# Kernel optimization log

Measured on AMD Instinct MI355X. Metric: run time of the kernel, lower is better.

Reference implementation:

```python
import jax, jax.numpy as jnp
import numpy as np

B, L = 16, 8192
D, NB, N, NC = 128, 6, 32, 16   # d_model, n_blocks, complex state modes (d_state//2), num_classes
E = 2 * D                       # FF expansion (expand=2)


def setup_inputs() -> dict:
    key = jax.random.key(0)
    ks = jax.random.split(key, 16)
    rn = lambda k, s, sc=0.02: jax.random.normal(k, s, jnp.float32) * sc
    return {
        "x": jax.random.normal(ks[0], (B, L, 1), jnp.float32),
        "conv_w": rn(ks[1], (D, 1, 5), 0.3),
        "conv_b": jnp.zeros((D,), jnp.float32),
        "s4_ln_w": jnp.ones((NB, D), jnp.float32),
        "s4_ln_b": jnp.zeros((NB, D), jnp.float32),
        "s4_log_dt": jax.random.uniform(ks[2], (NB, D), jnp.float32, np.log(1e-3), np.log(1e-1)),
        "s4_log_A_real": jnp.full((NB, D, N), np.log(0.5), jnp.float32),
        "s4_A_imag": jnp.ones((NB, D, 1), jnp.float32) * (np.pi * jnp.arange(N, dtype=jnp.float32)),
        "s4_C_re": rn(ks[3], (NB, D, N), 1.0),
        "s4_C_im": rn(ks[4], (NB, D, N), 1.0),
        "s4_D": rn(ks[5], (NB, D), 1.0),
        "s4_out_w": rn(ks[6], (NB, 2 * D, D)),
        "s4_out_b": jnp.zeros((NB, 2 * D), jnp.float32),
        "ff_ln_w": jnp.ones((NB, D), jnp.float32),
        "ff_ln_b": jnp.zeros((NB, D), jnp.float32),
        "ff_w1": rn(ks[7], (NB, E, D)),
        "ff_b1": jnp.zeros((NB, E), jnp.float32),
        "ff_w2": rn(ks[8], (NB, D, E)),
        "ff_b2": jnp.zeros((NB, D), jnp.float32),
        "head_w": rn(ks[9], (NC, D)),
        "head_b": jnp.zeros((NC,), jnp.float32),
    }


def _ln_c(h, w, b):
    # LayerNorm over channel dim of [B, D, L] (prenorm of ResidualBlock, transposed layout)
    mu = h.mean(1, keepdims=True)
    var = ((h - mu) ** 2).mean(1, keepdims=True)
    return (h - mu) * jax.lax.rsqrt(var + 1e-5) * w[None, :, None] + b[None, :, None]


def _s4(z, log_dt, log_A_real, A_imag, C_re, C_im, Dskip, out_w, out_b):
    # S4D diagonal SSM: ZOH-discretized kernel, FFT causal conv, GELU, GLU output projection
    Lq = z.shape[-1]
    dt = jnp.exp(log_dt)                                 # [D]
    A = -jnp.exp(log_A_real) + 1j * A_imag               # [D,N] stable diagonal
    dtA = dt[:, None] * A                                # [D,N]
    C = (C_re + 1j * C_im) * (jnp.exp(dtA) - 1.0) / A    # ZOH input discretization folded into C
    vand = jnp.exp(dtA[:, :, None] * jnp.arange(Lq))     # [D,N,L] Vandermonde of exp(dtA)
    K = 2.0 * jnp.einsum('dn,dnl->dl', C, vand).real     # [D,L] SSM convolution kernel
    nf = 2 * Lq
    y = jnp.fft.irfft(jnp.fft.rfft(z, n=nf) * jnp.fft.rfft(K, n=nf)[None], n=nf)[..., :Lq]
    y = jax.nn.gelu(y + Dskip[None, :, None] * z)        # skip term D*u then activation
    y = jnp.einsum('ed,bdl->bel', out_w, y) + out_b[None, :, None]  # position-wise d->2d
    a, g = jnp.split(y, 2, axis=1)
    return a * jax.nn.sigmoid(g)                          # GLU


def _logits(x, conv_w, conv_b, s4_ln_w, s4_ln_b, s4_log_dt, s4_log_A_real, s4_A_imag, s4_C_re, s4_C_im, s4_D, s4_out_w, s4_out_b, ff_ln_w, ff_ln_b, ff_w1, ff_b1, ff_w2, ff_b2, head_w, head_b):
    u = x.transpose(0, 2, 1)                             # [B,1,L]
    h = jax.lax.conv_general_dilated(u, conv_w, (1,), [(2, 2)], dimension_numbers=('NCH', 'OIH', 'NCH'))
    h = h + conv_b[None, :, None]                        # [B,D,L]
    nb = s4_log_dt.shape[0]
    for i in range(nb):
        z = _ln_c(h, s4_ln_w[i], s4_ln_b[i])
        h = h + _s4(z, s4_log_dt[i], s4_log_A_real[i], s4_A_imag[i], s4_C_re[i], s4_C_im[i], s4_D[i], s4_out_w[i], s4_out_b[i])
        z = _ln_c(h, ff_ln_w[i], ff_ln_b[i])
        z = jax.nn.gelu(jnp.einsum('ed,bdl->bel', ff_w1[i], z) + ff_b1[i][None, :, None])
        h = h + jnp.einsum('de,bel->bdl', ff_w2[i], z) + ff_b2[i][None, :, None]
    last = h[:, :, -1]                                   # take final timestep
    return last @ head_w.T + head_b                      # [B,NC]


def reference(x, conv_w, conv_b, s4_ln_w, s4_ln_b, s4_log_dt, s4_log_A_real, s4_A_imag, s4_C_re, s4_C_im, s4_D, s4_out_w, s4_out_b, ff_ln_w, ff_ln_b, ff_w1, ff_b1, ff_w2, ff_b2, head_w, head_b):
    logits = _logits(x, conv_w, conv_b, s4_ln_w, s4_ln_b, s4_log_dt, s4_log_A_real, s4_A_imag, s4_C_re, s4_C_im, s4_D, s4_out_w, s4_out_b, ff_ln_w, ff_ln_b, ff_w1, ff_b1, ff_w2, ff_b2, head_w, head_b)
    return jnp.argmax(logits, axis=-1)[:, None].astype(jnp.int32)
```

## Files before the change

kernel.cpp:

```cpp
#include <hip/hip_runtime.h>
#include <math.h>

#define Bb 16
#define Ls 8192
#define Dm 128
#define NBK 6
#define Nst 32
#define NCl 16
#define Em 256
#define LC 128
#define NCH 64
#define BL (Bb*Ls)

typedef __attribute__((ext_vector_type(8))) short bfrag;
typedef __attribute__((ext_vector_type(4))) float f32x4;

__device__ __forceinline__ float geluf(float x) {
    float x3 = x * x * x;
    float t = tanhf(fmaf(0.0356774081f, x3, 0.7978845608f * x));
    return 0.5f * x * (1.f + t);
}
__device__ __forceinline__ float sigmf(float x) { return 1.f / (1.f + expf(-x)); }

__device__ __forceinline__ unsigned short bf16r(float x) {
    unsigned u = __float_as_uint(x);
    return (unsigned short)((u + 0x7FFFu + ((u >> 16) & 1u)) >> 16);
}
__device__ __forceinline__ void split2(float x, unsigned short& h, unsigned short& l) {
    h = bf16r(x);
    float hf = __uint_as_float(((unsigned)h) << 16);
    l = bf16r(x - hf);
}

__global__ void s4e_conv(const float* __restrict__ x, const float* __restrict__ cw,
                         const float* __restrict__ cb, float* __restrict__ h) {
    int tid = blockIdx.x * 256 + threadIdx.x;
    int d4 = tid & 31;
    int t = tid >> 5;
    int l = t & (Ls - 1);
    int b = t >> 13;
    const float* xb = x + (size_t)b * Ls;
    float xs[5];
#pragma unroll
    for (int k = 0; k < 5; ++k) {
        int p = l + k - 2;
        xs[k] = (p >= 0 && p < Ls) ? xb[p] : 0.f;
    }
    float4 acc;
    float* ap = &acc.x;
#pragma unroll
    for (int j = 0; j < 4; ++j) {
        int d = d4 * 4 + j;
        float a = cb[d];
#pragma unroll
        for (int k = 0; k < 5; ++k) a = fmaf(cw[d * 5 + k], xs[k], a);
        ap[j] = a;
    }
    *(float4*)&h[(size_t)t * Dm + d4 * 4] = acc;
}

__global__ void s4e_lnstat(const float* __restrict__ h, float2* __restrict__ stats) {
    int tid = threadIdx.x;
    int t = blockIdx.x * 64 + (tid >> 2);
    int sub = tid & 3;
    const float* hp = h + (size_t)t * Dm + sub * 32;
    float s = 0.f, q = 0.f;
#pragma unroll
    for (int i = 0; i < 8; ++i) {
        float4 v = *(const float4*)(hp + i * 4);
        s += v.x + v.y + v.z + v.w;
        q += v.x * v.x + v.y * v.y + v.z * v.z + v.w * v.w;
    }
    s += __shfl_xor(s, 1); s += __shfl_xor(s, 2);
    q += __shfl_xor(q, 1); q += __shfl_xor(q, 2);
    float mu = s * (1.f / Dm);
    float rs = rsqrtf(q * (1.f / Dm) - mu * mu + 1e-5f);
    if (sub == 0) stats[t] = make_float2(mu, rs);
}

__global__ void s4e_setup(const float* __restrict__ log_dt, const float* __restrict__ lAr,
                          const float* __restrict__ Aim, const float* __restrict__ Cre,
                          const float* __restrict__ Cim, float2* __restrict__ wv,
                          float2* __restrict__ wp, float2* __restrict__ Cc) {
    int d = threadIdx.x;
    float dt = expf(log_dt[d]);
    for (int n = 0; n < Nst; ++n) {
        int id = d * Nst + n;
        float Ar = -expf(lAr[id]);
        float Ai = Aim[id];
        float xr = dt * Ar, xi = dt * Ai;
        float er = expf(xr);
        float wr = er * cosf(xi), wi = er * sinf(xi);
        wv[n * Dm + d] = make_float2(wr, wi);
        float den = Ar * Ar + Ai * Ai;
        float inv = 1.f / den;
        float fr = ((wr - 1.f) * Ar + wi * Ai) * inv;
        float fi = (wi * Ar - (wr - 1.f) * Ai) * inv;
        Cc[n * Dm + d] = make_float2(Cre[id] * fr - Cim[id] * fi, Cre[id] * fi + Cim[id] * fr);
        float pr = wr, pi = wi;
#pragma unroll
        for (int sq = 0; sq < 7; ++sq) {
            float nr = pr * pr - pi * pi;
            float ni = 2.f * pr * pi;
            pr = nr; pi = ni;
        }
        wp[n * Dm + d] = make_float2(pr, pi);
    }
}

__global__ void s4e_wsplit(const float* __restrict__ ow, const float* __restrict__ w1,
                           const float* __restrict__ w2, unsigned short* __restrict__ base) {
    int idx = blockIdx.x * 256 + threadIdx.x;
    int mat = idx >> 12;
    int g = idx & 4095;
    int lane = g & 63;
    int fid = g >> 6;
    int col = lane & 15, q = lane >> 4;
    const float* src;
    unsigned short *dh, *dl_;
    int rt, kt, K;
    if (mat == 0)      { src = ow; K = 128; dh = base;          dl_ = base + 32768;  rt = fid >> 2; kt = fid & 3; }
    else if (mat == 1) { src = w1; K = 128; dh = base + 65536;  dl_ = base + 98304;  rt = fid >> 2; kt = fid & 3; }
    else               { src = w2; K = 256; dh = base + 131072; dl_ = base + 163840; rt = fid >> 3; kt = fid & 7; }
    int row = rt * 16 + col;
    int k0 = kt * 32 + q * 8;
    const float* sp = src + row * K + k0;
    bfrag vh, vl;
#pragma unroll
    for (int j = 0; j < 8; ++j) {
        unsigned short hh, ll;
        split2(sp[j], hh, ll);
        vh[j] = (short)hh; vl[j] = (short)ll;
    }
    *(bfrag*)&dh[g * 8] = vh;
    *(bfrag*)&dl_[g * 8] = vl;
}

__global__ __launch_bounds__(256) void s4e_s1(const float* __restrict__ h,
        const float2* __restrict__ stats, const float* __restrict__ lnw,
        const float* __restrict__ lnb, const float2* __restrict__ wv,
        float2* __restrict__ send) {
    int tid = blockIdx.x * 256 + threadIdx.x;
    int dl = tid & 31;
    int m  = (tid >> 5) & 1;
    int dh = (tid >> 6) & 3;
    int c  = (tid >> 8) & (NCH - 1);
    int b  = tid >> 14;
    int d  = dh * 32 + dl;
    int n0 = m * 16;
    float wr[16], wi[16], sr[16], si[16];
#pragma unroll
    for (int k = 0; k < 16; ++k) {
        float2 t = wv[(n0 + k) * Dm + d];
        wr[k] = t.x; wi[k] = t.y; sr[k] = 0.f; si[k] = 0.f;
    }
    float wd = lnw[d], bd = lnb[d];
    const float* hp = h + ((size_t)b * Ls + c * LC) * Dm + d;
    const float2* st = stats + (size_t)b * Ls + c * LC;
#pragma unroll 4
    for (int j = 0; j < LC; ++j) {
        float2 sj = st[j];
        float zv = (hp[(size_t)j * Dm] - sj.x) * sj.y * wd + bd;
#pragma unroll
        for (int k = 0; k < 16; ++k) {
            float t = fmaf(-wi[k], si[k], zv);
            float nr = fmaf(wr[k], sr[k], t);
            float ni = fmaf(wi[k], sr[k], wr[k] * si[k]);
            sr[k] = nr; si[k] = ni;
        }
    }
    float2* o = send + ((size_t)(b * NCH + c) * Nst + n0) * Dm + d;
#pragma unroll
    for (int k = 0; k < 16; ++k) o[k * Dm] = make_float2(sr[k], si[k]);
}

__global__ void s4e_s2(const float2* __restrict__ wp, float2* __restrict__ s) {
    int tid = blockIdx.x * 256 + threadIdx.x;
    int d = tid & 127;
    int n = (tid >> 7) & 31;
    int b = tid >> 12;
    float2 W = wp[n * Dm + d];
    float Sr = 0.f, Si = 0.f;
    size_t base = ((size_t)(b * NCH) * Nst + n) * Dm + d;
    size_t cs = (size_t)Nst * Dm;
    for (int c0 = 0; c0 < NCH; c0 += 8) {
        float2 E[8];
#pragma unroll
        for (int k = 0; k < 8; ++k) E[k] = s[base + (size_t)(c0 + k) * cs];
#pragma unroll
        for (int k = 0; k < 8; ++k) {
            float2 o = make_float2(Sr, Si);
            float nr = fmaf(W.x, Sr, fmaf(-W.y, Si, E[k].x));
            float ni = fmaf(W.x, Si, fmaf(W.y, Sr, E[k].y));
            Sr = nr; Si = ni;
            s[base + (size_t)(c0 + k) * cs] = o;
        }
    }
}

__global__ __launch_bounds__(256) void s4e_s3(const float* __restrict__ h,
        const float2* __restrict__ stats, const float* __restrict__ lnw,
        const float* __restrict__ lnb, const float2* __restrict__ wv,
        const float2* __restrict__ Cc, const float2* __restrict__ sinit,
        const float* __restrict__ Dsk,
        unsigned short* __restrict__ acth, unsigned short* __restrict__ actl) {
    int tid = blockIdx.x * 256 + threadIdx.x;
    int dl = tid & 31;
    int m  = (tid >> 5) & 1;
    int dh = (tid >> 6) & 3;
    int c  = (tid >> 8) & (NCH - 1);
    int b  = tid >> 14;
    int d  = dh * 32 + dl;
    int n0 = m * 16;
    float wr[16], wi[16], cr[16], ci[16], sr[16], si[16];
    const float2* s0 = sinit + ((size_t)(b * NCH + c) * Nst + n0) * Dm + d;
#pragma unroll
    for (int k = 0; k < 16; ++k) {
        float2 t = wv[(n0 + k) * Dm + d];  wr[k] = t.x; wi[k] = t.y;
        float2 cc = Cc[(n0 + k) * Dm + d]; cr[k] = cc.x; ci[k] = cc.y;
        float2 ss = s0[k * Dm];            sr[k] = ss.x; si[k] = ss.y;
    }
    float wd = lnw[d], bd = lnb[d];
    float Dv = Dsk[d];
    size_t ib = ((size_t)b * Ls + c * LC) * Dm + d;
    const float2* st = stats + (size_t)b * Ls + c * LC;
#pragma unroll 2
    for (int j = 0; j < LC; ++j) {
        float2 sj = st[j];
        float zv = (h[ib + (size_t)j * Dm] - sj.x) * sj.y * wd + bd;
        float acc = 0.f;
#pragma unroll
        for (int k = 0; k < 16; ++k) {
            float t = fmaf(-wi[k], si[k], zv);
            float nr = fmaf(wr[k], sr[k], t);
            float ni = fmaf(wi[k], sr[k], wr[k] * si[k]);
            sr[k] = nr; si[k] = ni;
            acc = fmaf(cr[k], nr, acc);
            acc = fmaf(-ci[k], ni, acc);
        }
        acc += __shfl_xor(acc, 32);
        float av = geluf(fmaf(Dv, zv, 2.f * acc));
        unsigned short hh, ll;
        split2(av, hh, ll);
        if (m == 0) {
            acth[ib + (size_t)j * Dm] = hh;
            actl[ib + (size_t)j * Dm] = ll;
        }
    }
}

__global__ __launch_bounds__(256) void s4e_outproj(const unsigned short* __restrict__ acth,
        const unsigned short* __restrict__ actl, const unsigned short* __restrict__ wsp,
        const float* __restrict__ bias, float* __restrict__ h) {
    __shared__ __align__(16) unsigned short smem[8192];
    unsigned short* Ah = smem;
    unsigned short* Al = smem + 4096;
    float* Rf = (float*)smem;
    const unsigned short* Whi = wsp;
    const unsigned short* Wlo = wsp + 32768;
    size_t l0 = (size_t)blockIdx.x * 32;
    int tid = threadIdx.x;
    {
        const unsigned short* gh = acth + l0 * Dm;
        const unsigned short* gl = actl + l0 * Dm;
        for (int i = tid * 8; i < 32 * 128; i += 2048) {
            int r = i >> 7;
            int di = i ^ ((r & 7) << 3);
            *(bfrag*)&Ah[di] = *(const bfrag*)&gh[i];
            *(bfrag*)&Al[di] = *(const bfrag*)&gl[i];
        }
    }
    __syncthreads();
    int w = tid >> 6, lane = tid & 63;
    int col = lane & 15, q = lane >> 4;
    f32x4 acc[2][4];
#pragma unroll
    for (int m = 0; m < 2; ++m)
#pragma unroll
        for (int nt = 0; nt < 4; ++nt) acc[m][nt] = (f32x4){0.f, 0.f, 0.f, 0.f};
#pragma unroll
    for (int ks = 0; ks < 4; ++ks) {
        int kb = ks * 32 + q * 8;
        int i0 = (col * 128 + kb) ^ ((col & 7) << 3);
        int i1 = ((16 + col) * 128 + kb) ^ ((col & 7) << 3);
        bfrag a0h = *(bfrag*)&Ah[i0], a0l = *(bfrag*)&Al[i0];
        bfrag a1h = *(bfrag*)&Ah[i1], a1l = *(bfrag*)&Al[i1];
#pragma unroll
        for (int nt = 0; nt < 4; ++nt) {
            int rt = (nt < 2) ? (w * 2 + nt) : (8 + w * 2 + (nt - 2));
            int off = ((rt * 4 + ks) * 64 + lane) * 8;
            bfrag bh = *(const bfrag*)&Whi[off];
            bfrag bl = *(const bfrag*)&Wlo[off];
            acc[0][nt] = __builtin_amdgcn_mfma_f32_16x16x32_bf16(a0h, bh, acc[0][nt], 0, 0, 0);
            acc[0][nt] = __builtin_amdgcn_mfma_f32_16x16x32_bf16(a0h, bl, acc[0][nt], 0, 0, 0);
            acc[0][nt] = __builtin_amdgcn_mfma_f32_16x16x32_bf16(a0l, bh, acc[0][nt], 0, 0, 0);
            acc[1][nt] = __builtin_amdgcn_mfma_f32_16x16x32_bf16(a1h, bh, acc[1][nt], 0, 0, 0);
            acc[1][nt] = __builtin_amdgcn_mfma_f32_16x16x32_bf16(a1h, bl, acc[1][nt], 0, 0, 0);
            acc[1][nt] = __builtin_amdgcn_mfma_f32_16x16x32_bf16(a1l, bh, acc[1][nt], 0, 0, 0);
        }
    }
    __syncthreads();
#pragma unroll
    for (int m = 0; m < 2; ++m)
#pragma unroll
        for (int nt = 0; nt < 2; ++nt) {
            int dout = w * 32 + nt * 16 + col;
            float ba = bias[dout], bg = bias[dout + 128];
#pragma unroll
            for (int r = 0; r < 4; ++r) {
                int l = m * 16 + q * 4 + r;
                float a = acc[m][nt][r] + ba;
                float g = acc[m][nt + 2][r] + bg;
                Rf[l * 128 + dout] = a * sigmf(g);
            }
        }
    __syncthreads();
    size_t gb = l0 * Dm + (size_t)tid * 16;
#pragma unroll
    for (int i = 0; i < 4; ++i) {
        float4 r = *(float4*)&Rf[tid * 16 + i * 4];
        float4 hv = *(float4*)&h[gb + i * 4];
        hv.x += r.x; hv.y += r.y; hv.z += r.z; hv.w += r.w;
        *(float4*)&h[gb + i * 4] = hv;
    }
}

__global__ __launch_bounds__(256) void s4e_ffk(const float* __restrict__ lnw,
        const float* __restrict__ lnb, const unsigned short* __restrict__ wsp,
        const float* __restrict__ b1, const float* __restrict__ b2, float* __restrict__ h) {
    __shared__ __align__(16) unsigned short smem[24576];
    unsigned short* Zh = smem;
    unsigned short* Zl = smem + 4096;
    unsigned short* Eh = smem + 8192;
    unsigned short* El = smem + 16384;
    float* Rf = (float*)smem;
    const unsigned short* W1h = wsp + 65536;
    const unsigned short* W1l = wsp + 98304;
    const unsigned short* W2h = wsp + 131072;
    const unsigned short* W2l = wsp + 163840;
    size_t l0 = (size_t)blockIdx.x * 32;
    int tid = threadIdx.x;
    float hf[16];
    float s = 0.f, qq = 0.f;
    {
        const float* hp = h + l0 * Dm + (size_t)tid * 16;
#pragma unroll
        for (int i = 0; i < 4; ++i) {
            float4 v = *(const float4*)(hp + i * 4);
            hf[i * 4 + 0] = v.x; hf[i * 4 + 1] = v.y;
            hf[i * 4 + 2] = v.z; hf[i * 4 + 3] = v.w;
            s += v.x + v.y + v.z + v.w;
            qq += v.x * v.x + v.y * v.y + v.z * v.z + v.w * v.w;
        }
    }
    s  += __shfl_xor(s, 1);  s += __shfl_xor(s, 2);  s += __shfl_xor(s, 4);
    qq += __shfl_xor(qq, 1); qq += __shfl_xor(qq, 2); qq += __shfl_xor(qq, 4);
    float mu = s * (1.f / Dm);
    float rs = rsqrtf(qq * (1.f / Dm) - mu * mu + 1e-5f);
    int tok = tid >> 3, dc = (tid & 7) * 16;
#pragma unroll
    for (int g = 0; g < 2; ++g) {
        bfrag vh, vl;
#pragma unroll
        for (int k = 0; k < 8; ++k) {
            int d = dc + g * 8 + k;
            float v = (hf[g * 8 + k] - mu) * rs * lnw[d] + lnb[d];
            unsigned short hh, ll;
            split2(v, hh, ll);
            vh[k] = (short)hh; vl[k] = (short)ll;
        }
        int idx = (tok * 128 + dc + g * 8) ^ ((tok & 7) << 3);
        *(bfrag*)&Zh[idx] = vh;
        *(bfrag*)&Zl[idx] = vl;
    }
    __syncthreads();
    int w = tid >> 6, lane = tid & 63;
    int col = lane & 15, q = lane >> 4;
    f32x4 acc[2][4];
#pragma unroll
    for (int m = 0; m < 2; ++m)
#pragma unroll
        for (int nt = 0; nt < 4; ++nt) acc[m][nt] = (f32x4){0.f, 0.f, 0.f, 0.f};
#pragma unroll
    for (int ks = 0; ks < 4; ++ks) {
        int kb = ks * 32 + q * 8;
        int i0 = (col * 128 + kb) ^ ((col & 7) << 3);
        int i1 = ((16 + col) * 128 + kb) ^ ((col & 7) << 3);
        bfrag a0h = *(bfrag*)&Zh[i0], a0l = *(bfrag*)&Zl[i0];
        bfrag a1h = *(bfrag*)&Zh[i1], a1l = *(bfrag*)&Zl[i1];
#pragma unroll
        for (int nt = 0; nt < 4; ++nt) {
            int rt = w * 4 + nt;
            int off = ((rt * 4 + ks) * 64 + lane) * 8;
            bfrag bh = *(const bfrag*)&W1h[off];
            bfrag bl = *(const bfrag*)&W1l[off];
            acc[0][nt] = __builtin_amdgcn_mfma_f32_16x16x32_bf16(a0h, bh, acc[0][nt], 0, 0, 0);
            acc[0][nt] = __builtin_amdgcn_mfma_f32_16x16x32_bf16(a0h, bl, acc[0][nt], 0, 0, 0);
            acc[0][nt] = __builtin_amdgcn_mfma_f32_16x16x32_bf16(a0l, bh, acc[0][nt], 0, 0, 0);
            acc[1][nt] = __builtin_amdgcn_mfma_f32_16x16x32_bf16(a1h, bh, acc[1][nt], 0, 0, 0);
            acc[1][nt] = __builtin_amdgcn_mfma_f32_16x16x32_bf16(a1h, bl, acc[1][nt], 0, 0, 0);
            acc[1][nt] = __builtin_amdgcn_mfma_f32_16x16x32_bf16(a1l, bh, acc[1][nt], 0, 0, 0);
        }
    }
#pragma unroll
    for (int m = 0; m < 2; ++m)
#pragma unroll
        for (int nt = 0; nt < 4; ++nt) {
            int ei = w * 64 + nt * 16 + col;
            float bv = b1[ei];
#pragma unroll
            for (int r = 0; r < 4; ++r) {
                int l = m * 16 + q * 4 + r;
                float v = geluf(acc[m][nt][r] + bv);
                unsigned short hh, ll;
                split2(v, hh, ll);
                int idx = (l * 256 + ei) ^ ((l & 7) << 3);
                Eh[idx] = hh; El[idx] = ll;
            }
        }
    __syncthreads();
    f32x4 acc2[2][2];
#pragma unroll
    for (int m = 0; m < 2; ++m)
#pragma unroll
        for (int nt = 0; nt < 2; ++nt) acc2[m][nt] = (f32x4){0.f, 0.f, 0.f, 0.f};
#pragma unroll
    for (int ks = 0; ks < 8; ++ks) {
        int kb = ks * 32 + q * 8;
        int i0 = (col * 256 + kb) ^ ((col & 7) << 3);
        int i1 = ((16 + col) * 256 + kb) ^ ((col & 7) << 3);
        bfrag a0h = *(bfrag*)&Eh[i0], a0l = *(bfrag*)&El[i0];
        bfrag a1h = *(bfrag*)&Eh[i1], a1l = *(bfrag*)&El[i1];
#pragma unroll
        for (int nt = 0; nt < 2; ++nt) {
            int rt = w * 2 + nt;
            int off = ((rt * 8 + ks) * 64 + lane) * 8;
            bfrag bh = *(const bfrag*)&W2h[off];
            bfrag bl = *(const bfrag*)&W2l[off];
            acc2[0][nt] = __builtin_amdgcn_mfma_f32_16x16x32_bf16(a0h, bh, acc2[0][nt], 0, 0, 0);
            acc2[0][nt] = __builtin_amdgcn_mfma_f32_16x16x32_bf16(a0h, bl, acc2[0][nt], 0, 0, 0);
            acc2[0][nt] = __builtin_amdgcn_mfma_f32_16x16x32_bf16(a0l, bh, acc2[0][nt], 0, 0, 0);
            acc2[1][nt] = __builtin_amdgcn_mfma_f32_16x16x32_bf16(a1h, bh, acc2[1][nt], 0, 0, 0);
            acc2[1][nt] = __builtin_amdgcn_mfma_f32_16x16x32_bf16(a1h, bl, acc2[1][nt], 0, 0, 0);
            acc2[1][nt] = __builtin_amdgcn_mfma_f32_16x16x32_bf16(a1l, bh, acc2[1][nt], 0, 0, 0);
        }
    }
#pragma unroll
    for (int m = 0; m < 2; ++m)
#pragma unroll
        for (int nt = 0; nt < 2; ++nt) {
            int dout = w * 32 + nt * 16 + col;
            float bv = b2[dout];
#pragma unroll
            for (int r = 0; r < 4; ++r) {
                int l = m * 16 + q * 4 + r;
                Rf[l * 128 + dout] = acc2[m][nt][r] + bv;
            }
        }
    __syncthreads();
    size_t gb = l0 * Dm + (size_t)tid * 16;
#pragma unroll
    for (int i = 0; i < 4; ++i) {
        float4 r = *(float4*)&Rf[tid * 16 + i * 4];
        float4 o;
        o.x = hf[i * 4 + 0] + r.x; o.y = hf[i * 4 + 1] + r.y;
        o.z = hf[i * 4 + 2] + r.z; o.w = hf[i * 4 + 3] + r.w;
        *(float4*)&h[gb + i * 4] = o;
    }
}

__global__ void s4e_head(const float* __restrict__ h, const float* __restrict__ hw,
                         const float* __restrict__ hb, int* __restrict__ out) {
    __shared__ float logit[Bb][NCl];
    int tid = threadIdx.x;
    int b = tid >> 4, c = tid & 15;
    const float* hp = h + ((size_t)b * Ls + (Ls - 1)) * Dm;
    float acc = hb[c];
    for (int d = 0; d < Dm; ++d) acc = fmaf(hp[d], hw[c * Dm + d], acc);
    logit[b][c] = acc;
    __syncthreads();
    if (c == 0) {
        float best = logit[b][0]; int bi = 0;
#pragma unroll
        for (int k = 1; k < NCl; ++k) {
            float v = logit[b][k];
            if (v > best) { best = v; bi = k; }
        }
        out[b] = bi;
    }
}

extern "C" void kernel_launch(void* const* d_in, const int* in_sizes, int n_in,
                              void* d_out, int out_size, void* d_ws, size_t ws_size,
                              hipStream_t stream) {
    const float* x        = (const float*)d_in[0];
    const float* conv_w   = (const float*)d_in[1];
    const float* conv_b   = (const float*)d_in[2];
    const float* s4_ln_w  = (const float*)d_in[3];
    const float* s4_ln_b  = (const float*)d_in[4];
    const float* s4_logdt = (const float*)d_in[5];
    const float* s4_lAr   = (const float*)d_in[6];
    const float* s4_Aim   = (const float*)d_in[7];
    const float* s4_Cre   = (const float*)d_in[8];
    const float* s4_Cim   = (const float*)d_in[9];
    const float* s4_D     = (const float*)d_in[10];
    const float* s4_ow    = (const float*)d_in[11];
    const float* s4_ob    = (const float*)d_in[12];
    const float* ff_ln_w  = (const float*)d_in[13];
    const float* ff_ln_b  = (const float*)d_in[14];
    const float* ff_w1    = (const float*)d_in[15];
    const float* ff_b1    = (const float*)d_in[16];
    const float* ff_w2    = (const float*)d_in[17];
    const float* ff_b2    = (const float*)d_in[18];
    const float* head_w   = (const float*)d_in[19];
    const float* head_b   = (const float*)d_in[20];
    int* out = (int*)d_out;

    float* ws = (float*)d_ws;
    float* h  = ws;
    float2* stats = (float2*)(ws + 16777216);
    unsigned short* acth = (unsigned short*)(ws + 33554432);
    unsigned short* actl = (unsigned short*)(ws + 41943040);
    float2* send  = (float2*)(ws + 50331648);
    float2* wv    = (float2*)(ws + 58720256);
    float2* wp    = (float2*)(ws + 58728448);
    float2* Cc    = (float2*)(ws + 58736640);
    unsigned short* wsp = (unsigned short*)(ws + 58744832);

    s4e_conv<<<BL * 32 / 256, 256, 0, stream>>>(x, conv_w, conv_b, h);
    for (int i = 0; i < NBK; ++i) {
        s4e_setup<<<1, 128, 0, stream>>>(s4_logdt + i * Dm, s4_lAr + i * Dm * Nst,
                                         s4_Aim + i * Dm * Nst, s4_Cre + i * Dm * Nst,
                                         s4_Cim + i * Dm * Nst, wv, wp, Cc);
        s4e_wsplit<<<48, 256, 0, stream>>>(s4_ow + i * Em * Dm, ff_w1 + i * Em * Dm,
                                           ff_w2 + i * Dm * Em, wsp);
        s4e_lnstat<<<BL / 64, 256, 0, stream>>>(h, stats);
        s4e_s1<<<1024, 256, 0, stream>>>(h, stats, s4_ln_w + i * Dm, s4_ln_b + i * Dm, wv, send);
        s4e_s2<<<256, 256, 0, stream>>>(wp, send);
        s4e_s3<<<1024, 256, 0, stream>>>(h, stats, s4_ln_w + i * Dm, s4_ln_b + i * Dm,
                                         wv, Cc, send, s4_D + i * Dm, acth, actl);
        s4e_outproj<<<BL / 32, 256, 0, stream>>>(acth, actl, wsp, s4_ob + i * Em, h);
        s4e_ffk<<<BL / 32, 256, 0, stream>>>(ff_ln_w + i * Dm, ff_ln_b + i * Dm, wsp,
                                             ff_b1 + i * Em, ff_b2 + i * Dm, h);
    }
    s4e_head<<<1, 256, 0, stream>>>(h, head_w, head_b, out);
}
```

Before: 2.422 ms.

## Batch per-layer setup, stage LN stats in LDS, cheaper GELU in scan kernels

The per-layer parameter setup and weight-split kernels are replaced by single launches covering all six layers, which removes twelve small serialized launches from the layer loop. The scan kernels s1 and s3 now stage the chunk's LayerNorm statistics in shared memory and batch four h loads ahead of the recurrence. s3 computes GELU and the bf16 split only on the lanes that store the result, and the factor of 2 is folded into Cc. GELU switches to a sigmoid-form approximation built on exp2 and a hardware reciprocal, which slightly changes numerics.

```diff
diff --git a/kernel.cpp b/kernel.cpp
--- a/kernel.cpp
+++ b/kernel.cpp
@@ -16,11 +16,14 @@
 typedef __attribute__((ext_vector_type(4))) float f32x4;
 
 __device__ __forceinline__ float geluf(float x) {
-    float x3 = x * x * x;
-    float t = tanhf(fmaf(0.0356774081f, x3, 0.7978845608f * x));
-    return 0.5f * x * (1.f + t);
-}
-__device__ __forceinline__ float sigmf(float x) { return 1.f / (1.f + expf(-x)); }
+    float t = x * x;
+    float g = x * fmaf(0.102952207f, t, 2.30234547f);
+    float e = exp2f(-g);
+    return x * __builtin_amdgcn_rcpf(1.f + e);
+}
+__device__ __forceinline__ float sigmf(float x) {
+    return __builtin_amdgcn_rcpf(1.f + exp2f(-1.44269504f * x));
+}
 
 __device__ __forceinline__ unsigned short bf16r(float x) {
     unsigned u = __float_as_uint(x);
@@ -78,16 +81,25 @@
     if (sub == 0) stats[t] = make_float2(mu, rs);
 }
 
-__global__ void s4e_setup(const float* __restrict__ log_dt, const float* __restrict__ lAr,
-                          const float* __restrict__ Aim, const float* __restrict__ Cre,
-                          const float* __restrict__ Cim, float2* __restrict__ wv,
-                          float2* __restrict__ wp, float2* __restrict__ Cc) {
+__global__ void s4e_setup6(const float* __restrict__ log_dt, const float* __restrict__ lAr,
+                           const float* __restrict__ Aim, const float* __restrict__ Cre,
+                           const float* __restrict__ Cim, float2* __restrict__ wv6,
+                           float2* __restrict__ wp6, float2* __restrict__ Cc6) {
+    int i = blockIdx.x;
     int d = threadIdx.x;
-    float dt = expf(log_dt[d]);
+    const float* ld  = log_dt + i * Dm;
+    const float* la  = lAr + i * Dm * Nst;
+    const float* ai  = Aim + i * Dm * Nst;
+    const float* cre = Cre + i * Dm * Nst;
+    const float* cim = Cim + i * Dm * Nst;
+    float2* wv = wv6 + i * (Nst * Dm);
+    float2* wp = wp6 + i * (Nst * Dm);
+    float2* Cc = Cc6 + i * (Nst * Dm);
+    float dt = expf(ld[d]);
     for (int n = 0; n < Nst; ++n) {
         int id = d * Nst + n;
-        float Ar = -expf(lAr[id]);
-        float Ai = Aim[id];
+        float Ar = -expf(la[id]);
+        float Ai = ai[id];
         float xr = dt * Ar, xi = dt * Ai;
         float er = expf(xr);
         float wr = er * cosf(xi), wi = er * sinf(xi);
@@ -96,7 +108,8 @@
         float inv = 1.f / den;
         float fr = ((wr - 1.f) * Ar + wi * Ai) * inv;
         float fi = (wi * Ar - (wr - 1.f) * Ai) * inv;
-        Cc[n * Dm + d] = make_float2(Cre[id] * fr - Cim[id] * fi, Cre[id] * fi + Cim[id] * fr);
+        Cc[n * Dm + d] = make_float2(2.f * (cre[id] * fr - cim[id] * fi),
+                                     2.f * (cre[id] * fi + cim[id] * fr));
         float pr = wr, pi = wi;
 #pragma unroll
         for (int sq = 0; sq < 7; ++sq) {
@@ -108,20 +121,23 @@
     }
 }
 
-__global__ void s4e_wsplit(const float* __restrict__ ow, const float* __restrict__ w1,
-                           const float* __restrict__ w2, unsigned short* __restrict__ base) {
+__global__ void s4e_wsplit6(const float* __restrict__ ow, const float* __restrict__ w1,
+                            const float* __restrict__ w2, unsigned short* __restrict__ base0) {
     int idx = blockIdx.x * 256 + threadIdx.x;
-    int mat = idx >> 12;
-    int g = idx & 4095;
+    int layer = idx / 12288;
+    int r = idx - layer * 12288;
+    int mat = r >> 12;
+    int g = r & 4095;
     int lane = g & 63;
     int fid = g >> 6;
     int col = lane & 15, q = lane >> 4;
+    unsigned short* base = base0 + layer * 196608;
     const float* src;
     unsigned short *dh, *dl_;
     int rt, kt, K;
-    if (mat == 0)      { src = ow; K = 128; dh = base;          dl_ = base + 32768;  rt = fid >> 2; kt = fid & 3; }
-    else if (mat == 1) { src = w1; K = 128; dh = base + 65536;  dl_ = base + 98304;  rt = fid >> 2; kt = fid & 3; }
-    else               { src = w2; K = 256; dh = base + 131072; dl_ = base + 163840; rt = fid >> 3; kt = fid & 7; }
+    if (mat == 0)      { src = ow + layer * 32768; K = 128; dh = base;          dl_ = base + 32768;  rt = fid >> 2; kt = fid & 3; }
+    else if (mat == 1) { src = w1 + layer * 32768; K = 128; dh = base + 65536;  dl_ = base + 98304;  rt = fid >> 2; kt = fid & 3; }
+    else               { src = w2 + layer * 32768; K = 256; dh = base + 131072; dl_ = base + 163840; rt = fid >> 3; kt = fid & 7; }
     int row = rt * 16 + col;
     int k0 = kt * 32 + q * 8;
     const float* sp = src + row * K + k0;
@@ -140,14 +156,18 @@
         const float2* __restrict__ stats, const float* __restrict__ lnw,
         const float* __restrict__ lnb, const float2* __restrict__ wv,
         float2* __restrict__ send) {
-    int tid = blockIdx.x * 256 + threadIdx.x;
+    __shared__ float2 stl[LC];
+    int tid = threadIdx.x;
+    int blk = blockIdx.x;
+    int c = blk & (NCH - 1);
+    int b = blk >> 6;
     int dl = tid & 31;
     int m  = (tid >> 5) & 1;
-    int dh = (tid >> 6) & 3;
-    int c  = (tid >> 8) & (NCH - 1);
-    int b  = tid >> 14;
+    int dh = tid >> 6;
     int d  = dh * 32 + dl;
     int n0 = m * 16;
+    const float2* st = stats + (size_t)b * Ls + c * LC;
+    if (tid < LC) stl[tid] = st[tid];
     float wr[16], wi[16], sr[16], si[16];
 #pragma unroll
     for (int k = 0; k < 16; ++k) {
@@ -156,17 +176,28 @@
     }
     float wd = lnw[d], bd = lnb[d];
     const float* hp = h + ((size_t)b * Ls + c * LC) * Dm + d;
-    const float2* st = stats + (size_t)b * Ls + c * LC;
-#pragma unroll 4
-    for (int j = 0; j < LC; ++j) {
-        float2 sj = st[j];
-        float zv = (hp[(size_t)j * Dm] - sj.x) * sj.y * wd + bd;
-#pragma unroll
-        for (int k = 0; k < 16; ++k) {
-            float t = fmaf(-wi[k], si[k], zv);
-            float nr = fmaf(wr[k], sr[k], t);
-            float ni = fmaf(wi[k], sr[k], wr[k] * si[k]);
-            sr[k] = nr; si[k] = ni;
+    __syncthreads();
+#pragma unroll 1
+    for (int j = 0; j < LC; j += 4) {
+        float hv[4];
+#pragma unroll
+        for (int u = 0; u < 4; ++u) hv[u] = hp[(size_t)(j + u) * Dm];
+        float zv[4];
+#pragma unroll
+        for (int u = 0; u < 4; ++u) {
+            float2 sj = stl[j + u];
+            zv[u] = (hv[u] - sj.x) * sj.y * wd + bd;
+        }
+#pragma unroll
+        for (int u = 0; u < 4; ++u) {
+            float z = zv[u];
+#pragma unroll
+            for (int k = 0; k < 16; ++k) {
+                float t = fmaf(-wi[k], si[k], z);
+                float nr = fmaf(wr[k], sr[k], t);
+                float ni = fmaf(wi[k], sr[k], wr[k] * si[k]);
+                sr[k] = nr; si[k] = ni;
+            }
         }
     }
     float2* o = send + ((size_t)(b * NCH + c) * Nst + n0) * Dm + d;
@@ -204,14 +235,18 @@
         const float2* __restrict__ Cc, const float2* __restrict__ sinit,
         const float* __restrict__ Dsk,
         unsigned short* __restrict__ acth, unsigned short* __restrict__ actl) {
-    int tid = blockIdx.x * 256 + threadIdx.x;
+    __shared__ float2 stl[LC];
+    int tid = threadIdx.x;
+    int blk = blockIdx.x;
+    int c = blk & (NCH - 1);
+    int b = blk >> 6;
     int dl = tid & 31;
     int m  = (tid >> 5) & 1;
-    int dh = (tid >> 6) & 3;
-    int c  = (tid >> 8) & (NCH - 1);
-    int b  = tid >> 14;
+    int dh = tid >> 6;
     int d  = dh * 32 + dl;
     int n0 = m * 16;
+    const float2* st = stats + (size_t)b * Ls + c * LC;
+    if (tid < LC) stl[tid] = st[tid];
     float wr[16], wi[16], cr[16], ci[16], sr[16], si[16];
     const float2* s0 = sinit + ((size_t)(b * NCH + c) * Nst + n0) * Dm + d;
 #pragma unroll
@@ -223,28 +258,39 @@
     float wd = lnw[d], bd = lnb[d];
     float Dv = Dsk[d];
     size_t ib = ((size_t)b * Ls + c * LC) * Dm + d;
-    const float2* st = stats + (size_t)b * Ls + c * LC;
-#pragma unroll 2
-    for (int j = 0; j < LC; ++j) {
-        float2 sj = st[j];
-        float zv = (h[ib + (size_t)j * Dm] - sj.x) * sj.y * wd + bd;
-        float acc = 0.f;
-#pragma unroll
-        for (int k = 0; k < 16; ++k) {
-            float t = fmaf(-wi[k], si[k], zv);
-            float nr = fmaf(wr[k], sr[k], t);
-            float ni = fmaf(wi[k], sr[k], wr[k] * si[k]);
-            sr[k] = nr; si[k] = ni;
-            acc = fmaf(cr[k], nr, acc);
-            acc = fmaf(-ci[k], ni, acc);
-        }
-        acc += __shfl_xor(acc, 32);
-        float av = geluf(fmaf(Dv, zv, 2.f * acc));
-        unsigned short hh, ll;
-        split2(av, hh, ll);
-        if (m == 0) {
-            acth[ib + (size_t)j * Dm] = hh;
-            actl[ib + (size_t)j * Dm] = ll;
+    __syncthreads();
+#pragma unroll 1
+    for (int j = 0; j < LC; j += 4) {
+        float hv[4];
+#pragma unroll
+        for (int u = 0; u < 4; ++u) hv[u] = h[ib + (size_t)(j + u) * Dm];
+        float zv[4];
+#pragma unroll
+        for (int u = 0; u < 4; ++u) {
+            float2 sj = stl[j + u];
+            zv[u] = (hv[u] - sj.x) * sj.y * wd + bd;
+        }
+#pragma unroll
+        for (int u = 0; u < 4; ++u) {
+            float z = zv[u];
+            float acc = 0.f;
+#pragma unroll
+            for (int k = 0; k < 16; ++k) {
+                float t = fmaf(-wi[k], si[k], z);
+                float nr = fmaf(wr[k], sr[k], t);
+                float ni = fmaf(wi[k], sr[k], wr[k] * si[k]);
+                sr[k] = nr; si[k] = ni;
+                acc = fmaf(cr[k], nr, acc);
+                acc = fmaf(-ci[k], ni, acc);
+            }
+            acc += __shfl_xor(acc, 32);
+            if (m == 0) {
+                float av = geluf(fmaf(Dv, z, acc));
+                unsigned short hh, ll;
+                split2(av, hh, ll);
+                acth[ib + (size_t)(j + u) * Dm] = hh;
+                actl[ib + (size_t)(j + u) * Dm] = ll;
+            }
         }
     }
 }
@@ -519,21 +565,23 @@
     float* ws = (float*)d_ws;
     float* h  = ws;
     float2* stats = (float2*)(ws + 16777216);
+    float2* wv6 = (float2*)(ws + 17039360);
+    float2* wp6 = (float2*)(ws + 17088512);
+    float2* Cc6 = (float2*)(ws + 17137664);
+    unsigned short* wsp6 = (unsigned short*)(ws + 17186816);
     unsigned short* acth = (unsigned short*)(ws + 33554432);
     unsigned short* actl = (unsigned short*)(ws + 41943040);
     float2* send  = (float2*)(ws + 50331648);
-    float2* wv    = (float2*)(ws + 58720256);
-    float2* wp    = (float2*)(ws + 58728448);
-    float2* Cc    = (float2*)(ws + 58736640);
-    unsigned short* wsp = (unsigned short*)(ws + 58744832);
 
     s4e_conv<<<BL * 32 / 256, 256, 0, stream>>>(x, conv_w, conv_b, h);
+    s4e_setup6<<<NBK, 128, 0, stream>>>(s4_logdt, s4_lAr, s4_Aim, s4_Cre, s4_Cim,
+                                        wv6, wp6, Cc6);
+    s4e_wsplit6<<<288, 256, 0, stream>>>(s4_ow, ff_w1, ff_w2, wsp6);
     for (int i = 0; i < NBK; ++i) {
-        s4e_setup<<<1, 128, 0, stream>>>(s4_logdt + i * Dm, s4_lAr + i * Dm * Nst,
-                                         s4_Aim + i * Dm * Nst, s4_Cre + i * Dm * Nst,
-                                         s4_Cim + i * Dm * Nst, wv, wp, Cc);
-        s4e_wsplit<<<48, 256, 0, stream>>>(s4_ow + i * Em * Dm, ff_w1 + i * Em * Dm,
-                                           ff_w2 + i * Dm * Em, wsp);
+        float2* wv = wv6 + i * (Nst * Dm);
+        float2* wp = wp6 + i * (Nst * Dm);
+        float2* Cc = Cc6 + i * (Nst * Dm);
+        unsigned short* wsp = wsp6 + i * 196608;
         s4e_lnstat<<<BL / 64, 256, 0, stream>>>(h, stats);
         s4e_s1<<<1024, 256, 0, stream>>>(h, stats, s4_ln_w + i * Dm, s4_ln_b + i * Dm, wv, send);
         s4e_s2<<<256, 256, 0, stream>>>(wp, send);
```

Result: faster. 2.132 ms (-12.0%).
